# Kernel optimization log

Measured on AMD Instinct MI355X. Metric: run time of the kernel, lower is better.

## Reference

```python
import jax, jax.numpy as jnp
import numpy as np

N = 50000
E = 800000
IN_C = 64
OUT_C = 64
EPS = 1 + 1e-06


def setup_inputs() -> dict:
    key = jax.random.key(0)
    ks = jax.random.split(key, 10)
    x = jax.random.normal(ks[0], (N, IN_C), dtype=jnp.float32)
    lower_indices = jax.random.randint(ks[1], (2, E), 0, N, dtype=jnp.int64)
    lower_values = jax.random.uniform(ks[2], (E,), dtype=jnp.float32)
    upper_indices = jax.random.randint(ks[3], (2, E), 0, N, dtype=jnp.int64)
    upper_values = jax.random.uniform(ks[4], (E,), dtype=jnp.float32)
    s = 1.0 / np.sqrt(IN_C)
    w_lower = jax.random.uniform(ks[5], (IN_C, OUT_C), jnp.float32, -s, s)
    a_lower = jax.random.uniform(ks[6], (2 * OUT_C,), jnp.float32, -s, s)
    w_upper = jax.random.uniform(ks[7], (IN_C, OUT_C), jnp.float32, -s, s)
    a_upper = jax.random.uniform(ks[8], (2 * OUT_C,), jnp.float32, -s, s)
    w_lin = jax.random.uniform(ks[9], (IN_C, OUT_C), jnp.float32, -s, s)
    return {
        "x": x,
        "lower_indices": lower_indices,
        "lower_values": lower_values,
        "upper_indices": upper_indices,
        "upper_values": upper_values,
        "w_lower": w_lower,
        "a_lower": a_lower,
        "w_upper": w_upper,
        "a_upper": a_upper,
        "w_lin": w_lin,
    }


def _att_conv(x, weight, att_w, indices, values):
    """TopoModelX base Conv with att=True.

    x_msg = x @ weight; per edge (i=target, j=source):
      alpha_e = elu(concat(x_msg[j], x_msg[i]) @ att_w) * nbhd_vals_e
    out[i] = sum_e alpha_e * x_msg[j]
    """
    xm = x @ weight                              # [N, out]
    i, j = indices[0], indices[1]                # target, source
    # concat(src, tgt) @ a == src @ a[:F] + tgt @ a[F:]; precompute per-node
    s_src = xm @ att_w[:OUT_C]                   # [N]
    s_tgt = xm @ att_w[OUT_C:]                   # [N]
    alpha = jax.nn.elu(s_src[j] + s_tgt[i]) * values   # [E]
    msg = alpha[:, None] * xm[j]                 # [E, out]
    return jax.ops.segment_sum(msg, i, num_segments=N)


def reference(x, lower_indices, lower_values, upper_indices, upper_values,
              w_lower, a_lower, w_upper, a_upper, w_lin):
    lower_x = _att_conv(x, w_lower, a_lower, lower_indices, lower_values)
    upper_x = _att_conv(x, w_upper, a_upper, upper_indices, upper_values)
    w_x = (x @ w_lin) * EPS
    # Aggregation(aggr_func='sum', update_func='relu')
    return jax.nn.relu(lower_x + upper_x + w_x)
```

## Files before the change

kernel.cpp:

```cpp
#include <hip/hip_runtime.h>
#include <hip/hip_bf16.h>
#include <math.h>

#define N_NODES 50000
#define N_EDGES 800000
#define C 64
#define EPS_F 1.000001f

#define CAPN 48
#define OVF_IDX 0
#define OMAX 4096
#define LOVF 64

#define RB_BITS 7
#define RBUK (1 << RB_BITS)
#define NBUCK (2 * N_NODES)
#define NREG ((NBUCK + RBUK - 1) >> RB_BITS)
#define RCAP 2560
#define EPB 8192
#define NP1 ((2 * N_EDGES + EPB - 1) / EPB)
#define NPREB 784
#define NK1 (NP1 + NPREB)

#define ZERON (1 + NREG)

#define NPRE ((N_NODES + 31) / 32)

typedef __attribute__((ext_vector_type(8))) unsigned short u16x8;

__device__ __forceinline__ unsigned short f2bf(float f) {
    unsigned u = __float_as_uint(f);
    return (unsigned short)((u + 0x7FFFu + ((u >> 16) & 1u)) >> 16);
}
__device__ __forceinline__ float bf2f(unsigned short b) {
    return __uint_as_float(((unsigned)b) << 16);
}

__global__ __launch_bounds__(256) void s_kernel(
    const float* __restrict__ x,
    const float* __restrict__ w_l, const float* __restrict__ a_l,
    const float* __restrict__ w_u, const float* __restrict__ a_u,
    float* __restrict__ ssl, float* __restrict__ stl,
    float* __restrict__ ssu, float* __restrict__ stu,
    int* __restrict__ cnt)
{
    const int b = blockIdx.x;
    const int t = threadIdx.x;

    const int gz = b * 256 + t;
    if (gz < ZERON) cnt[gz] = 0;

    __shared__ float wa[4 * C];
    {
        const int v = t >> 6;
        const int k = t & 63;
        const float* __restrict__ w = (v < 2) ? w_l : w_u;
        const float* __restrict__ a = (v < 2) ? a_l : a_u;
        const int ao = (v & 1) * C;
        float acc = 0.f;
#pragma unroll 16
        for (int o = 0; o < C; ++o)
            acc = fmaf(w[k * C + o], a[ao + o], acc);
        wa[v * C + k] = acc;
    }
    __syncthreads();

    const int lane = t & 63;
    const int wv = t >> 6;
    const int row0 = b * 32 + wv * 8;
    if (row0 >= N_NODES) return;

    const float wls = wa[lane], wlt = wa[C + lane];
    const float wus = wa[2 * C + lane], wut = wa[3 * C + lane];

#pragma unroll
    for (int r = 0; r < 8; ++r) {
        const int row = row0 + r;
        if (row >= N_NODES) break;
        const float xv = x[row * C + lane];
        float psl = xv * wls, ptl = xv * wlt;
        float psu = xv * wus, ptu = xv * wut;
#pragma unroll
        for (int o = 32; o >= 1; o >>= 1) {
            psl += __shfl_xor(psl, o);
            ptl += __shfl_xor(ptl, o);
            psu += __shfl_xor(psu, o);
            ptu += __shfl_xor(ptu, o);
        }
        if (lane == 0) {
            ssl[row] = psl; stl[row] = ptl;
            ssu[row] = psu; stu[row] = ptu;
        }
    }
}

__global__ __launch_bounds__(512) void gemm_scatter_kernel(
    const float* __restrict__ x,
    const float* __restrict__ w_l, const float* __restrict__ w_u,
    const float* __restrict__ w_lin,
    const int* __restrict__ lidx, const float* __restrict__ lval,
    const int* __restrict__ uidx, const float* __restrict__ uval,
    const float* __restrict__ ssl, const float* __restrict__ stl,
    const float* __restrict__ ssu, const float* __restrict__ stu,
    unsigned short* __restrict__ xm_l, unsigned short* __restrict__ xm_u,
    float* __restrict__ xlin,
    int* __restrict__ cnt, uint2* __restrict__ rbuf, int2* __restrict__ ovf)
{
    const int b = blockIdx.x, t = threadIdx.x;
    __shared__ int hist[NREG];

    if (b % 5 == 0) {
        const int p = b / 5;
        int* __restrict__ rcur = cnt + 1;

        for (int s0 = t; s0 < NREG; s0 += 512) hist[s0] = 0;
        __syncthreads();

        unsigned lo[16];
        int bk[16];
        const int gbase = p * EPB + t;
#pragma unroll
        for (int k = 0; k < 16; ++k) {
            const int g = gbase + k * 512;
            bk[k] = -1;
            if (g < 2 * N_EDGES) {
                int i, j;
                float v, s;
                if (g < N_EDGES) {
                    i = lidx[g]; j = lidx[N_EDGES + g]; v = lval[g];
                    s = ssl[j] + stl[i];
                    bk[k] = 2 * i;
                } else {
                    const int e = g - N_EDGES;
                    i = uidx[e]; j = uidx[N_EDGES + e]; v = uval[e];
                    s = ssu[j] + stu[i];
                    bk[k] = 2 * i + 1;
                }
                s = (s > 0.f) ? s : expm1f(s);
                lo[k] = ((unsigned)j << 16) | (unsigned)f2bf(s * v);
                atomicAdd(&hist[bk[k] >> RB_BITS], 1);
            }
        }
        __syncthreads();

        for (int cb = t; cb < NREG; cb += 512) {
            const int c = hist[cb];
            hist[cb] = c ? atomicAdd(&rcur[cb], c) : 0;
        }
        __syncthreads();

#pragma unroll
        for (int k = 0; k < 16; ++k) {
            if (bk[k] >= 0) {
                const int cb = bk[k] >> RB_BITS;
                const int slot = atomicAdd(&hist[cb], 1);
                if (slot < RCAP) {
                    rbuf[(size_t)cb * RCAP + slot] = make_uint2(lo[k], (unsigned)bk[k]);
                } else {
                    const int oi = atomicAdd(&cnt[OVF_IDX], 1);
                    if (oi < OMAX) ovf[oi] = make_int2(bk[k], (int)lo[k]);
                }
            }
        }
        return;
    }

    const int pid = b - b / 5 - 1;
    const int lane = t & 63;
    const int wvu = __builtin_amdgcn_readfirstlane(t >> 6);
    const int row0 = pid * 64 + wvu * 8;
    if (row0 >= N_NODES) return;

    const float* xr[8];
#pragma unroll
    for (int r = 0; r < 8; ++r) {
        int rr = row0 + r;
        if (rr >= N_NODES) rr = N_NODES - 1;
        xr[r] = x + (size_t)rr * C;
    }

    float acc_l[8] = {0,0,0,0,0,0,0,0};
    float acc_u[8] = {0,0,0,0,0,0,0,0};
    float acc_n[8] = {0,0,0,0,0,0,0,0};

#pragma unroll 1
    for (int kc = 0; kc < C; kc += 4) {
#pragma unroll
        for (int kk = 0; kk < 4; ++kk) {
            const int k = kc + kk;
            const float wl = w_l[k * C + lane];
            const float wu = w_u[k * C + lane];
            const float wn = w_lin[k * C + lane];
#pragma unroll
            for (int r = 0; r < 8; ++r) {
                const float xk = xr[r][k];
                acc_l[r] = fmaf(xk, wl, acc_l[r]);
                acc_u[r] = fmaf(xk, wu, acc_u[r]);
                acc_n[r] = fmaf(xk, wn, acc_n[r]);
            }
        }
    }

#pragma unroll
    for (int r = 0; r < 8; ++r) {
        const int row = row0 + r;
        if (row < N_NODES) {
            xm_l[row * C + lane] = f2bf(acc_l[r]);
            xm_u[row * C + lane] = f2bf(acc_u[r]);
            xlin[row * C + lane] = acc_n[r] * EPS_F;
        }
    }
}

__global__ __launch_bounds__(512) void gather_kernel(
    const float* __restrict__ xlin,
    const int* __restrict__ cnt, const uint2* __restrict__ rbuf,
    const int2* __restrict__ ovf,
    const unsigned short* __restrict__ xm_l, const unsigned short* __restrict__ xm_u,
    float* __restrict__ out)
{
    const int cb = blockIdx.x;
    const int t = threadIdx.x;
    const int wv = t >> 6, lane = t & 63;
    const int sub8 = lane >> 3;
    const int cg = lane & 7;

    __shared__ unsigned lists[RBUK * CAPN];
    __shared__ int cur[RBUK];
    __shared__ int lovf_bk[LOVF];
    __shared__ unsigned lovf_rc[LOVF];
    __shared__ int lc;

    for (int s0 = t; s0 < RBUK; s0 += 512) cur[s0] = 0;
    if (t == 0) lc = 0;
    __syncthreads();

    const int n = min(cnt[1 + cb], RCAP);
    const uint2* __restrict__ rb = rbuf + (size_t)cb * RCAP;
    for (int r = t; r < n; r += 512) {
        const uint2 e = rb[r];
        const int local = (int)e.y & (RBUK - 1);
        const int rank = atomicAdd(&cur[local], 1);
        if (rank < CAPN) {
            lists[local * CAPN + rank] = e.x;
        } else {
            const int o = atomicAdd(&lc, 1);
            if (o < LOVF) { lovf_bk[o] = local; lovf_rc[o] = e.x; }
        }
    }
    __syncthreads();

    const int oc = min(cnt[OVF_IDX], OMAX);
    const int lc2 = min(lc, LOVF);

#pragma unroll 1
    for (int p = 0; p < 8; ++p) {
        const int q = wv * 8 + p;
        const int node = cb * 64 + q;
        if (node >= N_NODES) break;
        const int lA = 2 * q, lB = 2 * q + 1;
        const int lenA = min(cur[lA], CAPN);
        const int lenB = min(cur[lB], CAPN);
        const unsigned* __restrict__ lstA = lists + lA * CAPN;
        const unsigned* __restrict__ lstB = lists + lB * CAPN;

        float acc[8] = {0.f,0.f,0.f,0.f,0.f,0.f,0.f,0.f};
        int kA = 0, kB = 0;
        while ((kA < lenA) | (kB < lenB)) {
            const int iA = kA + sub8, iB = kB + sub8;
            const bool aA = iA < lenA, aB = iB < lenB;
            const unsigned rwA = lstA[aA ? iA : kA];
            const unsigned rwB = lstB[aB ? iB : kB];
            const int jA = aA ? (int)(rwA >> 16) : 0;
            const int jB = aB ? (int)(rwB >> 16) : 0;
            const float wA = aA ? bf2f((unsigned short)(rwA & 0xFFFFu)) : 0.f;
            const float wB = aB ? bf2f((unsigned short)(rwB & 0xFFFFu)) : 0.f;
            const u16x8 rowA = *(const u16x8*)(xm_l + jA * C + cg * 8);
            const u16x8 rowB = *(const u16x8*)(xm_u + jB * C + cg * 8);
#pragma unroll
            for (int c = 0; c < 8; ++c)
                acc[c] = fmaf(wA, bf2f(rowA[c]), acc[c]);
#pragma unroll
            for (int c = 0; c < 8; ++c)
                acc[c] = fmaf(wB, bf2f(rowB[c]), acc[c]);
            kA += (kA < lenA) ? 8 : 0;
            kB += (kB < lenB) ? 8 : 0;
        }

        for (int u = 0; u < oc; ++u) {
            const int2 e = ovf[u];
            if (e.x == 2 * node || e.x == 2 * node + 1) {
                const unsigned rw = (unsigned)e.y;
                const int j = (int)(rw >> 16);
                const float w = (sub8 == 0) ? bf2f((unsigned short)(rw & 0xFFFFu)) : 0.f;
                const unsigned short* xm = (e.x & 1) ? xm_u : xm_l;
                const u16x8 row = *(const u16x8*)(xm + j * C + cg * 8);
#pragma unroll
                for (int c = 0; c < 8; ++c)
                    acc[c] = fmaf(w, bf2f(row[c]), acc[c]);
            }
        }

        for (int u = 0; u < lc2; ++u) {
            const int bkl = lovf_bk[u];
            if (bkl == lA || bkl == lB) {
                const unsigned rw = lovf_rc[u];
                const int j = (int)(rw >> 16);
                const float w = (sub8 == 0) ? bf2f((unsigned short)(rw & 0xFFFFu)) : 0.f;
                const unsigned short* xm = (bkl & 1) ? xm_u : xm_l;
                const u16x8 row = *(const u16x8*)(xm + j * C + cg * 8);
#pragma unroll
                for (int c = 0; c < 8; ++c)
                    acc[c] = fmaf(w, bf2f(row[c]), acc[c]);
            }
        }

#pragma unroll
        for (int o = 8; o <= 32; o <<= 1)
#pragma unroll
            for (int c = 0; c < 8; ++c)
                acc[c] += __shfl_xor(acc[c], o);

        if (lane < 8) {
            const float* __restrict__ xl = xlin + (size_t)node * C + lane * 8;
            const float4 xa = *(const float4*)(xl);
            const float4 xb = *(const float4*)(xl + 4);
            float4 oa, ob;
            oa.x = fmaxf(acc[0] + xa.x, 0.f);
            oa.y = fmaxf(acc[1] + xa.y, 0.f);
            oa.z = fmaxf(acc[2] + xa.z, 0.f);
            oa.w = fmaxf(acc[3] + xa.w, 0.f);
            ob.x = fmaxf(acc[4] + xb.x, 0.f);
            ob.y = fmaxf(acc[5] + xb.y, 0.f);
            ob.z = fmaxf(acc[6] + xb.z, 0.f);
            ob.w = fmaxf(acc[7] + xb.w, 0.f);
            float* __restrict__ op = out + (size_t)node * C + lane * 8;
            *(float4*)(op) = oa;
            *(float4*)(op + 4) = ob;
        }
    }
}

extern "C" void kernel_launch(void* const* d_in, const int* in_sizes, int n_in,
                              void* d_out, int out_size, void* d_ws, size_t ws_size,
                              hipStream_t stream)
{
    const float* x          = (const float*)d_in[0];
    const int*   lower_idx  = (const int*)d_in[1];
    const float* lower_vals = (const float*)d_in[2];
    const int*   upper_idx  = (const int*)d_in[3];
    const float* upper_vals = (const float*)d_in[4];
    const float* w_lower    = (const float*)d_in[5];
    const float* a_lower    = (const float*)d_in[6];
    const float* w_upper    = (const float*)d_in[7];
    const float* a_upper    = (const float*)d_in[8];
    const float* w_lin      = (const float*)d_in[9];

    float* out = (float*)d_out;
    char* ws = (char*)d_ws;

    const size_t NC_F = (size_t)N_NODES * C * sizeof(float);
    const size_t NC_H = (size_t)N_NODES * C * sizeof(unsigned short);
    unsigned short* xm_l = (unsigned short*)ws;  ws += NC_H;
    unsigned short* xm_u = (unsigned short*)ws;  ws += NC_H;
    float* xlin = (float*)ws;                 ws += NC_F;
    float* ssl  = (float*)ws;                 ws += N_NODES * sizeof(float);
    float* stl  = (float*)ws;                 ws += N_NODES * sizeof(float);
    float* ssu  = (float*)ws;                 ws += N_NODES * sizeof(float);
    float* stu  = (float*)ws;                 ws += N_NODES * sizeof(float);
    int2* ovf   = (int2*)ws;                  ws += OMAX * sizeof(int2);
    uint2* rbuf = (uint2*)ws;                 ws += (size_t)NREG * RCAP * sizeof(uint2);
    int* cnt    = (int*)ws;                   ws += (size_t)(ZERON + 32) * sizeof(int);

    s_kernel<<<NPRE, 256, 0, stream>>>(
        x, w_lower, a_lower, w_upper, a_upper,
        ssl, stl, ssu, stu, cnt);

    gemm_scatter_kernel<<<NK1, 512, 0, stream>>>(
        x, w_lower, w_upper, w_lin,
        lower_idx, lower_vals, upper_idx, upper_vals,
        ssl, stl, ssu, stu,
        xm_l, xm_u, xlin, cnt, rbuf, ovf);

    gather_kernel<<<NREG, 512, 0, stream>>>(
        xlin, cnt, rbuf, ovf, xm_l, xm_u, out);
}
```

Measured before the change: 193.1 us.

## Split scatter pass into histogram-then-compute loops and reorder block assignment

The edge-partition blocks no longer keep 16 packed edges in registers across the histogram barrier. A first loop reads only the target indices to build the bucket histogram, and a second loop re-reads the edge data to compute the attention weights and scatter into bucket slots. Launch bounds now request 4 blocks per CU, and partition blocks are placed first in the grid instead of every fifth block. This is meant to cut register pressure and raise occupancy, at the cost of reading the index arrays twice.

After: 199.9 us. +3.5%, slower.

```diff
diff --git a/kernel.cpp b/kernel.cpp
--- a/kernel.cpp
+++ b/kernel.cpp
@@ -94,7 +94,7 @@
     }
 }
 
-__global__ __launch_bounds__(512) void gemm_scatter_kernel(
+__global__ __launch_bounds__(512, 4) void gemm_scatter_kernel(
     const float* __restrict__ x,
     const float* __restrict__ w_l, const float* __restrict__ w_u,
     const float* __restrict__ w_lin,
@@ -109,63 +109,64 @@
     const int b = blockIdx.x, t = threadIdx.x;
     __shared__ int hist[NREG];
 
-    if (b % 5 == 0) {
-        const int p = b / 5;
+    if (b < NP1) {
+        const int p = b;
         int* __restrict__ rcur = cnt + 1;
 
         for (int s0 = t; s0 < NREG; s0 += 512) hist[s0] = 0;
         __syncthreads();
 
-        unsigned lo[16];
-        int bk[16];
         const int gbase = p * EPB + t;
-#pragma unroll
+
+#pragma unroll 4
         for (int k = 0; k < 16; ++k) {
             const int g = gbase + k * 512;
-            bk[k] = -1;
             if (g < 2 * N_EDGES) {
-                int i, j;
+                const int bk = (g < N_EDGES) ? (2 * lidx[g])
+                                             : (2 * uidx[g - N_EDGES] + 1);
+                atomicAdd(&hist[bk >> RB_BITS], 1);
+            }
+        }
+        __syncthreads();
+
+        for (int cb = t; cb < NREG; cb += 512) {
+            const int c = hist[cb];
+            hist[cb] = c ? atomicAdd(&rcur[cb], c) : 0;
+        }
+        __syncthreads();
+
+#pragma unroll 4
+        for (int k = 0; k < 16; ++k) {
+            const int g = gbase + k * 512;
+            if (g < 2 * N_EDGES) {
+                int i, j, bk;
                 float v, s;
                 if (g < N_EDGES) {
                     i = lidx[g]; j = lidx[N_EDGES + g]; v = lval[g];
                     s = ssl[j] + stl[i];
-                    bk[k] = 2 * i;
+                    bk = 2 * i;
                 } else {
                     const int e = g - N_EDGES;
                     i = uidx[e]; j = uidx[N_EDGES + e]; v = uval[e];
                     s = ssu[j] + stu[i];
-                    bk[k] = 2 * i + 1;
+                    bk = 2 * i + 1;
                 }
                 s = (s > 0.f) ? s : expm1f(s);
-                lo[k] = ((unsigned)j << 16) | (unsigned)f2bf(s * v);
-                atomicAdd(&hist[bk[k] >> RB_BITS], 1);
-            }
-        }
-        __syncthreads();
-
-        for (int cb = t; cb < NREG; cb += 512) {
-            const int c = hist[cb];
-            hist[cb] = c ? atomicAdd(&rcur[cb], c) : 0;
-        }
-        __syncthreads();
-
-#pragma unroll
-        for (int k = 0; k < 16; ++k) {
-            if (bk[k] >= 0) {
-                const int cb = bk[k] >> RB_BITS;
+                const unsigned lo = ((unsigned)j << 16) | (unsigned)f2bf(s * v);
+                const int cb = bk >> RB_BITS;
                 const int slot = atomicAdd(&hist[cb], 1);
                 if (slot < RCAP) {
-                    rbuf[(size_t)cb * RCAP + slot] = make_uint2(lo[k], (unsigned)bk[k]);
+                    rbuf[(size_t)cb * RCAP + slot] = make_uint2(lo, (unsigned)bk);
                 } else {
                     const int oi = atomicAdd(&cnt[OVF_IDX], 1);
-                    if (oi < OMAX) ovf[oi] = make_int2(bk[k], (int)lo[k]);
+                    if (oi < OMAX) ovf[oi] = make_int2(bk, (int)lo);
                 }
             }
         }
         return;
     }
 
-    const int pid = b - b / 5 - 1;
+    const int pid = b - NP1;
     const int lane = t & 63;
     const int wvu = __builtin_amdgcn_readfirstlane(t >> 6);
     const int row0 = pid * 64 + wvu * 8;
```

## Fold attention score computation into GEMM and defer ELU weighting to gather

Applied to the files above, without the earlier changes.

Removes the separate score kernel. Per-node source and target attention scores are now computed in the GEMM epilogue from the fp32 accumulators, and the counter reset becomes a memset. The scatter phase now stores only the raw edge value. The gather kernel looks up ssl/ssu for each source, adds the target score and applies the ELU per edge. This saves one launch and the score lookups in the scatter phase, at the cost of extra random scalar loads and expm1 calls in the gather loop. Scores now come from unrounded xm rather than a precomputed W·a product, which slightly changes numerics.

Measured after the change: 174.5 us. -9.6%, faster.

```diff
diff --git a/kernel.cpp b/kernel.cpp
--- a/kernel.cpp
+++ b/kernel.cpp
@@ -24,8 +24,6 @@
 
 #define ZERON (1 + NREG)
 
-#define NPRE ((N_NODES + 31) / 32)
-
 typedef __attribute__((ext_vector_type(8))) unsigned short u16x8;
 
 __device__ __forceinline__ unsigned short f2bf(float f) {
@@ -36,74 +34,17 @@
     return __uint_as_float(((unsigned)b) << 16);
 }
 
-__global__ __launch_bounds__(256) void s_kernel(
+__global__ __launch_bounds__(512) void gemm_scatter_kernel(
     const float* __restrict__ x,
     const float* __restrict__ w_l, const float* __restrict__ a_l,
     const float* __restrict__ w_u, const float* __restrict__ a_u,
-    float* __restrict__ ssl, float* __restrict__ stl,
-    float* __restrict__ ssu, float* __restrict__ stu,
-    int* __restrict__ cnt)
-{
-    const int b = blockIdx.x;
-    const int t = threadIdx.x;
-
-    const int gz = b * 256 + t;
-    if (gz < ZERON) cnt[gz] = 0;
-
-    __shared__ float wa[4 * C];
-    {
-        const int v = t >> 6;
-        const int k = t & 63;
-        const float* __restrict__ w = (v < 2) ? w_l : w_u;
-        const float* __restrict__ a = (v < 2) ? a_l : a_u;
-        const int ao = (v & 1) * C;
-        float acc = 0.f;
-#pragma unroll 16
-        for (int o = 0; o < C; ++o)
-            acc = fmaf(w[k * C + o], a[ao + o], acc);
-        wa[v * C + k] = acc;
-    }
-    __syncthreads();
-
-    const int lane = t & 63;
-    const int wv = t >> 6;
-    const int row0 = b * 32 + wv * 8;
-    if (row0 >= N_NODES) return;
-
-    const float wls = wa[lane], wlt = wa[C + lane];
-    const float wus = wa[2 * C + lane], wut = wa[3 * C + lane];
-
-#pragma unroll
-    for (int r = 0; r < 8; ++r) {
-        const int row = row0 + r;
-        if (row >= N_NODES) break;
-        const float xv = x[row * C + lane];
-        float psl = xv * wls, ptl = xv * wlt;
-        float psu = xv * wus, ptu = xv * wut;
-#pragma unroll
-        for (int o = 32; o >= 1; o >>= 1) {
-            psl += __shfl_xor(psl, o);
-            ptl += __shfl_xor(ptl, o);
-            psu += __shfl_xor(psu, o);
-            ptu += __shfl_xor(ptu, o);
-        }
-        if (lane == 0) {
-            ssl[row] = psl; stl[row] = ptl;
-            ssu[row] = psu; stu[row] = ptu;
-        }
-    }
-}
-
-__global__ __launch_bounds__(512) void gemm_scatter_kernel(
-    const float* __restrict__ x,
-    const float* __restrict__ w_l, const float* __restrict__ w_u,
     const float* __restrict__ w_lin,
     const int* __restrict__ lidx, const float* __restrict__ lval,
     const int* __restrict__ uidx, const float* __restrict__ uval,
-    const float* __restrict__ ssl, const float* __restrict__ stl,
-    const float* __restrict__ ssu, const float* __restrict__ stu,
     unsigned short* __restrict__ xm_l, unsigned short* __restrict__ xm_u,
     float* __restrict__ xlin,
+    float* __restrict__ ssl, float* __restrict__ stl,
+    float* __restrict__ ssu, float* __restrict__ stu,
     int* __restrict__ cnt, uint2* __restrict__ rbuf, int2* __restrict__ ovf)
 {
     const int b = blockIdx.x, t = threadIdx.x;
@@ -125,19 +66,16 @@
             bk[k] = -1;
             if (g < 2 * N_EDGES) {
                 int i, j;
-                float v, s;
+                float v;
                 if (g < N_EDGES) {
                     i = lidx[g]; j = lidx[N_EDGES + g]; v = lval[g];
-                    s = ssl[j] + stl[i];
                     bk[k] = 2 * i;
                 } else {
                     const int e = g - N_EDGES;
                     i = uidx[e]; j = uidx[N_EDGES + e]; v = uval[e];
-                    s = ssu[j] + stu[i];
                     bk[k] = 2 * i + 1;
                 }
-                s = (s > 0.f) ? s : expm1f(s);
-                lo[k] = ((unsigned)j << 16) | (unsigned)f2bf(s * v);
+                lo[k] = ((unsigned)j << 16) | (unsigned)f2bf(v);
                 atomicAdd(&hist[bk[k] >> RB_BITS], 1);
             }
         }
@@ -201,6 +139,9 @@
         }
     }
 
+    const float als = a_l[lane], alt = a_l[C + lane];
+    const float aus = a_u[lane], aut = a_u[C + lane];
+
 #pragma unroll
     for (int r = 0; r < 8; ++r) {
         const int row = row0 + r;
@@ -208,6 +149,20 @@
             xm_l[row * C + lane] = f2bf(acc_l[r]);
             xm_u[row * C + lane] = f2bf(acc_u[r]);
             xlin[row * C + lane] = acc_n[r] * EPS_F;
+
+            float psl = acc_l[r] * als, ptl = acc_l[r] * alt;
+            float psu = acc_u[r] * aus, ptu = acc_u[r] * aut;
+#pragma unroll
+            for (int o = 32; o >= 1; o >>= 1) {
+                psl += __shfl_xor(psl, o);
+                ptl += __shfl_xor(ptl, o);
+                psu += __shfl_xor(psu, o);
+                ptu += __shfl_xor(ptu, o);
+            }
+            if (lane == 0) {
+                ssl[row] = psl; stl[row] = ptl;
+                ssu[row] = psu; stu[row] = ptu;
+            }
         }
     }
 }
@@ -217,6 +172,8 @@
     const int* __restrict__ cnt, const uint2* __restrict__ rbuf,
     const int2* __restrict__ ovf,
     const unsigned short* __restrict__ xm_l, const unsigned short* __restrict__ xm_u,
+    const float* __restrict__ ssl, const float* __restrict__ stl,
+    const float* __restrict__ ssu, const float* __restrict__ stu,
     float* __restrict__ out)
 {
     const int cb = blockIdx.x;
@@ -264,6 +221,9 @@
         const unsigned* __restrict__ lstA = lists + lA * CAPN;
         const unsigned* __restrict__ lstB = lists + lB * CAPN;
 
+        const float stlN = stl[node];
+        const float stuN = stu[node];
+
         float acc[8] = {0.f,0.f,0.f,0.f,0.f,0.f,0.f,0.f};
         int kA = 0, kB = 0;
         while ((kA < lenA) | (kB < lenB)) {
@@ -273,8 +233,14 @@
             const unsigned rwB = lstB[aB ? iB : kB];
             const int jA = aA ? (int)(rwA >> 16) : 0;
             const int jB = aB ? (int)(rwB >> 16) : 0;
-            const float wA = aA ? bf2f((unsigned short)(rwA & 0xFFFFu)) : 0.f;
-            const float wB = aB ? bf2f((unsigned short)(rwB & 0xFFFFu)) : 0.f;
+            const float vA = aA ? bf2f((unsigned short)(rwA & 0xFFFFu)) : 0.f;
+            const float vB = aB ? bf2f((unsigned short)(rwB & 0xFFFFu)) : 0.f;
+            const float sA = ssl[jA] + stlN;
+            const float sB = ssu[jB] + stuN;
+            const float eA = (sA > 0.f) ? sA : expm1f(sA);
+            const float eB = (sB > 0.f) ? sB : expm1f(sB);
+            const float wA = eA * vA;
+            const float wB = eB * vB;
             const u16x8 rowA = *(const u16x8*)(xm_l + jA * C + cg * 8);
             const u16x8 rowB = *(const u16x8*)(xm_u + jB * C + cg * 8);
 #pragma unroll
@@ -292,8 +258,12 @@
             if (e.x == 2 * node || e.x == 2 * node + 1) {
                 const unsigned rw = (unsigned)e.y;
                 const int j = (int)(rw >> 16);
-                const float w = (sub8 == 0) ? bf2f((unsigned short)(rw & 0xFFFFu)) : 0.f;
-                const unsigned short* xm = (e.x & 1) ? xm_u : xm_l;
+                const float v = bf2f((unsigned short)(rw & 0xFFFFu));
+                const int cv = e.x & 1;
+                const float s = (cv ? ssu[j] : ssl[j]) + (cv ? stuN : stlN);
+                const float el = (s > 0.f) ? s : expm1f(s);
+                const float w = (sub8 == 0) ? el * v : 0.f;
+                const unsigned short* xm = cv ? xm_u : xm_l;
                 const u16x8 row = *(const u16x8*)(xm + j * C + cg * 8);
 #pragma unroll
                 for (int c = 0; c < 8; ++c)
@@ -306,8 +276,12 @@
             if (bkl == lA || bkl == lB) {
                 const unsigned rw = lovf_rc[u];
                 const int j = (int)(rw >> 16);
-                const float w = (sub8 == 0) ? bf2f((unsigned short)(rw & 0xFFFFu)) : 0.f;
-                const unsigned short* xm = (bkl & 1) ? xm_u : xm_l;
+                const float v = bf2f((unsigned short)(rw & 0xFFFFu));
+                const int cv = bkl & 1;
+                const float s = (cv ? ssu[j] : ssl[j]) + (cv ? stuN : stlN);
+                const float el = (s > 0.f) ? s : expm1f(s);
+                const float w = (sub8 == 0) ? el * v : 0.f;
+                const unsigned short* xm = cv ? xm_u : xm_l;
                 const u16x8 row = *(const u16x8*)(xm + j * C + cg * 8);
 #pragma unroll
                 for (int c = 0; c < 8; ++c)
@@ -372,16 +346,13 @@
     uint2* rbuf = (uint2*)ws;                 ws += (size_t)NREG * RCAP * sizeof(uint2);
     int* cnt    = (int*)ws;                   ws += (size_t)(ZERON + 32) * sizeof(int);
 
-    s_kernel<<<NPRE, 256, 0, stream>>>(
-        x, w_lower, a_lower, w_upper, a_upper,
-        ssl, stl, ssu, stu, cnt);
+    hipMemsetAsync(cnt, 0, ZERON * sizeof(int), stream);
 
     gemm_scatter_kernel<<<NK1, 512, 0, stream>>>(
-        x, w_lower, w_upper, w_lin,
+        x, w_lower, a_lower, w_upper, a_upper, w_lin,
         lower_idx, lower_vals, upper_idx, upper_vals,
-        ssl, stl, ssu, stu,
-        xm_l, xm_u, xlin, cnt, rbuf, ovf);
+        xm_l, xm_u, xlin, ssl, stl, ssu, stu, cnt, rbuf, ovf);
 
     gather_kernel<<<NREG, 512, 0, stream>>>(
-        xlin, cnt, rbuf, ovf, xm_l, xm_u, out);
-}
+        xlin, cnt, rbuf, ovf, xm_l, xm_u, ssl, stl, ssu, stu, out);
+}
```
